# Performance work log

Hardware: AMD Instinct MI355X
Metric: run time of the kernel (lower is better)

The kernel has to match this reference:

```python
import jax, jax.numpy as jnp
import numpy as np

S, B, D, H, F = 1024, 8, 1024, 16, 4096
HD = D // H
EPS = 1e-5


def setup_inputs() -> dict:
    key = jax.random.key(0)
    ks = jax.random.split(key, 12)
    sc_d = 1.0 / np.sqrt(D)
    sc_f = 1.0 / np.sqrt(F)
    return {
        "src": jax.random.normal(ks[0], (S, B, D), jnp.float32),
        "in_proj_w": jax.random.uniform(ks[1], (3 * D, D), jnp.float32, -sc_d, sc_d),
        "in_proj_b": jnp.zeros((3 * D,), jnp.float32),
        "out_w": jax.random.uniform(ks[2], (D, D), jnp.float32, -sc_d, sc_d),
        "out_b": jnp.zeros((D,), jnp.float32),
        "w1": jax.random.uniform(ks[3], (F, D), jnp.float32, -sc_d, sc_d),
        "b1": jax.random.uniform(ks[4], (F,), jnp.float32, -sc_d, sc_d),
        "w2": jax.random.uniform(ks[5], (D, F), jnp.float32, -sc_f, sc_f),
        "b2": jax.random.uniform(ks[6], (D,), jnp.float32, -sc_f, sc_f),
        "g1": jnp.ones((D,), jnp.float32),
        "be1": jnp.zeros((D,), jnp.float32),
        "g2": jnp.ones((D,), jnp.float32),
        "be2": jnp.zeros((D,), jnp.float32),
    }


def _layer_norm(x, g, b):
    mu = jnp.mean(x, axis=-1, keepdims=True)
    var = jnp.mean(jnp.square(x - mu), axis=-1, keepdims=True)
    return (x - mu) * jax.lax.rsqrt(var + EPS) * g + b


def reference(src, in_proj_w, in_proj_b, out_w, out_b, w1, b1, w2, b2, g1, be1, g2, be2):
    wq, wk, wv = jnp.split(in_proj_w, 3, axis=0)
    bq, bk, bv = jnp.split(in_proj_b, 3, axis=0)
    scale = 1.0 / np.sqrt(HD)
    # src: [S, B, D] -> q/k/v: [S, B, H, HD]
    q = (src @ wq.T + bq).reshape(S, B, H, HD) * scale
    k = (src @ wk.T + bk).reshape(S, B, H, HD)
    v = (src @ wv.T + bv).reshape(S, B, H, HD)
    # full score matrix [B, H, S, S] (matches the unfused bmm/softmax/bmm)
    scores = jnp.einsum("sbhd,tbhd->bhst", q, k)
    attn = jax.nn.softmax(scores, axis=-1)
    ctx = jnp.einsum("bhst,tbhd->sbhd", attn, v).reshape(S, B, D)
    attn_out = ctx @ out_w.T + out_b
    x = _layer_norm(src + attn_out, g1, be1)
    ffn = jax.nn.relu(x @ w1.T + b1) @ w2.T + b2
    return _layer_norm(x + ffn, g2, be2)
```

## Files before the change

### kernel.cpp

```cpp
#include <hip/hip_runtime.h>
#include <hip/hip_bf16.h>
#include <stdint.h>

typedef __bf16 bf16x8 __attribute__((ext_vector_type(8)));
typedef __bf16 bf16x4 __attribute__((ext_vector_type(4)));
typedef float floatx4 __attribute__((ext_vector_type(4)));

typedef __attribute__((address_space(1))) void gvoid;
typedef __attribute__((address_space(3))) void lvoid;

__device__ __forceinline__ void async_load16(const __bf16* g, __bf16* l) {
  __builtin_amdgcn_global_load_lds((gvoid*)g, (lvoid*)l, 16, 0, 0);
}

__device__ __forceinline__ bf16x8 ld8(const float* p) {
  const floatx4 a = *(const floatx4*)p;
  const floatx4 b = *(const floatx4*)(p + 4);
  bf16x8 r;
  r[0] = (__bf16)a[0]; r[1] = (__bf16)a[1];
  r[2] = (__bf16)a[2]; r[3] = (__bf16)a[3];
  r[4] = (__bf16)b[0]; r[5] = (__bf16)b[1];
  r[6] = (__bf16)b[2]; r[7] = (__bf16)b[3];
  return r;
}

__global__ __launch_bounds__(256) void cvt_kernel(const float* __restrict__ in,
                                                  __bf16* __restrict__ out,
                                                  int n) {
  const int i = (blockIdx.x * 256 + threadIdx.x) * 8;
  if (i < n) *(bf16x8*)(out + i) = ld8(in + i);
}

template <int EPI>
__global__ __launch_bounds__(256, 2) void gemm_db64(
    const __bf16* __restrict__ A, const __bf16* __restrict__ Bt,
    const float* __restrict__ bias, const float* __restrict__ resf,
    const __bf16* __restrict__ resb, __bf16* __restrict__ o0,
    __bf16* __restrict__ o2, int M, int N, int K, int ldb) {
  __shared__ __align__(16) __bf16 As[2][2][128 * 32];
  __shared__ __align__(16) __bf16 Bs[2][2][128 * 32];
  const int tid = threadIdx.x;
  const int w = tid >> 6;
  const int lane = tid & 63;
  const int l16 = lane & 15;
  const int quad = lane >> 4;
  const int wm = (w & 1) * 64;
  const int wn = (w >> 1) * 64;
  const int bm = blockIdx.y * 128;
  const int bn = blockIdx.x * 128;

  floatx4 acc[4][4];
#pragma unroll
  for (int i = 0; i < 4; ++i)
#pragma unroll
    for (int j = 0; j < 4; ++j) acc[i][j] = (floatx4){0.f, 0.f, 0.f, 0.f};

  const int arow = lane >> 2, acol = (lane & 3) * 8;
  const __bf16* Ag = A + (int64_t)(bm + w * 32 + arow) * K + acol;
  const __bf16* Bg = Bt + (int64_t)(bn + w * 32 + arow) * ldb + acol;

  auto STAGE = [&](int b, int k0) {
#pragma unroll
    for (int kh = 0; kh < 2; ++kh) {
      __bf16* AsW = As[b][kh] + (w * 32) * 32;
      async_load16(Ag + k0 + kh * 32, AsW);
      async_load16(Ag + k0 + kh * 32 + 16 * K, AsW + 16 * 32);
      __bf16* BsW = Bs[b][kh] + (w * 32) * 32;
      async_load16(Bg + k0 + kh * 32, BsW);
      async_load16(Bg + k0 + kh * 32 + 16 * ldb, BsW + 16 * 32);
    }
  };

  STAGE(0, 0);
  __syncthreads();

  int cur = 0;
  for (int k0 = 0; k0 < K; k0 += 64) {
    if (k0 + 64 < K) STAGE(cur ^ 1, k0 + 64);
#pragma unroll
    for (int kh = 0; kh < 2; ++kh) {
      bf16x8 af[4], bfr[4];
#pragma unroll
      for (int i = 0; i < 4; ++i) {
        af[i] = *(const bf16x8*)(As[cur][kh] + (wm + i * 16 + l16) * 32 + quad * 8);
        bfr[i] = *(const bf16x8*)(Bs[cur][kh] + (wn + i * 16 + l16) * 32 + quad * 8);
      }
#pragma unroll
      for (int mi = 0; mi < 4; ++mi)
#pragma unroll
        for (int ni = 0; ni < 4; ++ni)
          acc[mi][ni] = __builtin_amdgcn_mfma_f32_16x16x32_bf16(
              af[mi], bfr[ni], acc[mi][ni], 0, 0, 0);
    }
    __syncthreads();
    cur ^= 1;
  }

#pragma unroll
  for (int ni = 0; ni < 4; ++ni) {
    const int gn = bn + wn + ni * 16 + l16;
    const float bv = (EPI == 3) ? 0.f : bias[gn];
#pragma unroll
    for (int mi = 0; mi < 4; ++mi) {
#pragma unroll
      for (int r = 0; r < 4; ++r) {
        const int gm = bm + wm + mi * 16 + quad * 4 + r;
        float v = acc[mi][ni][r] + bv;
        if (EPI == 0) {
          if (gn < 2048) {
            o0[(int64_t)gm * 2048 + gn] = (__bf16)(gn < 1024 ? v * 0.125f : v);
          } else {
            const int nn = gn - 2048, hh = nn >> 6, d = nn & 63;
            const int s = gm >> 3, b = gm & 7;
            o2[((b * 16 + hh) * 64 + d) * 1024 + s] = (__bf16)v;
          }
        } else {
          if (EPI == 1) v += resf[(int64_t)gm * N + gn];
          if (EPI == 3 || EPI == 4) v += (float)resb[(int64_t)gm * N + gn];
          if (EPI == 2) v = fmaxf(v, 0.f);
          o0[(int64_t)gm * N + gn] = (__bf16)v;
        }
      }
    }
  }
}

constexpr int BM = 128, BN = 128, BK = 32;

template <typename AT, int EPI>
__global__ __launch_bounds__(256, 2) void gemm_db(
    const AT* __restrict__ A, const __bf16* __restrict__ Bt,
    const float* __restrict__ bias, const float* __restrict__ resf,
    const __bf16* __restrict__ resb, __bf16* __restrict__ o0,
    __bf16* __restrict__ o2, int M, int N, int K, int ldb) {
  constexpr bool AF = sizeof(AT) == 4;
  __shared__ __align__(16) __bf16 As[2][BM * BK];
  __shared__ __align__(16) __bf16 Bs[2][BN * BK];
  const int tid = threadIdx.x;
  const int w = tid >> 6;
  const int lane = tid & 63;
  const int l16 = lane & 15;
  const int quad = lane >> 4;
  const int wm = (w & 1) * 64;
  const int wn = (w >> 1) * 64;
  const int bm = blockIdx.y * BM;
  const int bn = blockIdx.x * BN;

  floatx4 acc[4][4];
#pragma unroll
  for (int i = 0; i < 4; ++i)
#pragma unroll
    for (int j = 0; j < 4; ++j) acc[i][j] = (floatx4){0.f, 0.f, 0.f, 0.f};

  const int srow = tid >> 2, scol = (tid & 3) * 8;
  const int arow = lane >> 2, acol = (lane & 3) * 8;
  const AT* Ag;
  if constexpr (AF) Ag = A + (int64_t)(bm + srow) * K + scol;
  else Ag = A + (int64_t)(bm + w * 32 + arow) * K + acol;
  const __bf16* Bg = Bt + (int64_t)(bn + w * 32 + arow) * ldb + acol;

  bf16x8 a0, a1;
  if constexpr (AF) {
    a0 = ld8(Ag);
    a1 = ld8(Ag + (int64_t)64 * K);
    *(bf16x8*)(As[0] + tid * 8) = a0;
    *(bf16x8*)(As[0] + 2048 + tid * 8) = a1;
    if (BK < K) {
      a0 = ld8(Ag + BK);
      a1 = ld8(Ag + BK + (int64_t)64 * K);
    }
  } else {
    __bf16* AsW = As[0] + (w * 32) * BK;
    async_load16(Ag, AsW);
    async_load16(Ag + 16 * K, AsW + 16 * BK);
  }
  {
    __bf16* BsW = Bs[0] + (w * 32) * BK;
    async_load16(Bg, BsW);
    async_load16(Bg + 16 * ldb, BsW + 16 * BK);
  }
  __syncthreads();

  int cur = 0;
  for (int k0 = 0; k0 < K; k0 += BK) {
    const bool more = (k0 + BK) < K;
    if (more) {
      if constexpr (AF) {
        *(bf16x8*)(As[cur ^ 1] + tid * 8) = a0;
        *(bf16x8*)(As[cur ^ 1] + 2048 + tid * 8) = a1;
        if (k0 + 2 * BK < K) {
          a0 = ld8(Ag + k0 + 2 * BK);
          a1 = ld8(Ag + k0 + 2 * BK + (int64_t)64 * K);
        }
      } else {
        __bf16* AsW = As[cur ^ 1] + (w * 32) * BK;
        async_load16(Ag + k0 + BK, AsW);
        async_load16(Ag + k0 + BK + 16 * K, AsW + 16 * BK);
      }
      __bf16* BsW = Bs[cur ^ 1] + (w * 32) * BK;
      async_load16(Bg + k0 + BK, BsW);
      async_load16(Bg + k0 + BK + 16 * ldb, BsW + 16 * BK);
    }
    bf16x8 af[4], bfr[4];
#pragma unroll
    for (int i = 0; i < 4; ++i) {
      af[i] = *(const bf16x8*)(As[cur] + (wm + i * 16 + l16) * BK + quad * 8);
      bfr[i] = *(const bf16x8*)(Bs[cur] + (wn + i * 16 + l16) * BK + quad * 8);
    }
#pragma unroll
    for (int mi = 0; mi < 4; ++mi)
#pragma unroll
      for (int ni = 0; ni < 4; ++ni)
        acc[mi][ni] = __builtin_amdgcn_mfma_f32_16x16x32_bf16(
            af[mi], bfr[ni], acc[mi][ni], 0, 0, 0);
    __syncthreads();
    cur ^= 1;
  }

#pragma unroll
  for (int ni = 0; ni < 4; ++ni) {
    const int gn = bn + wn + ni * 16 + l16;
    const float bv = (EPI == 3) ? 0.f : bias[gn];
#pragma unroll
    for (int mi = 0; mi < 4; ++mi) {
#pragma unroll
      for (int r = 0; r < 4; ++r) {
        const int gm = bm + wm + mi * 16 + quad * 4 + r;
        float v = acc[mi][ni][r] + bv;
        if (EPI == 0) {
          if (gn < 2048) {
            o0[(int64_t)gm * 2048 + gn] = (__bf16)(gn < 1024 ? v * 0.125f : v);
          } else {
            const int nn = gn - 2048, hh = nn >> 6, d = nn & 63;
            const int s = gm >> 3, b = gm & 7;
            o2[((b * 16 + hh) * 64 + d) * 1024 + s] = (__bf16)v;
          }
        } else {
          if (EPI == 1) v += resf[(int64_t)gm * N + gn];
          if (EPI == 3 || EPI == 4) v += (float)resb[(int64_t)gm * N + gn];
          if (EPI == 2) v = fmaxf(v, 0.f);
          o0[(int64_t)gm * N + gn] = (__bf16)v;
        }
      }
    }
  }
}

__global__ __launch_bounds__(256) void attn_flash(
    const __bf16* __restrict__ qk, const __bf16* __restrict__ vT,
    __bf16* __restrict__ ctx) {
  constexpr int S = 1024, PSTR = 36;
  constexpr int ROWSTR = 8 * 2048;
  __shared__ __align__(16) __bf16 Kb[2][2048];
  __shared__ __align__(16) __bf16 Vb[2][2048];
  __shared__ __align__(16) __bf16 Pt[4][32 * PSTR];
  const int tid = threadIdx.x;
  const int w = tid >> 6;
  const int lane = tid & 63;
  const int l16 = lane & 15;
  const int quad = lane >> 4;
  const int bh = blockIdx.y, bidx = bh >> 4, h = bh & 15;
  const int qbase = blockIdx.x * 128 + w * 32;

  const __bf16* qp =
      qk + ((int64_t)(qbase + l16) * 8 + bidx) * 2048 + h * 64 + quad * 8;
  bf16x8 aq[2][2];
  aq[0][0] = *(const bf16x8*)qp;
  aq[0][1] = *(const bf16x8*)(qp + 32);
  aq[1][0] = *(const bf16x8*)(qp + 16 * ROWSTR);
  aq[1][1] = *(const bf16x8*)(qp + 16 * ROWSTR + 32);

  const __bf16* kg = qk + 1024 +
      ((int64_t)((w >> 1) * 16 + l16) * 8 + bidx) * 2048 + h * 64 +
      ((w & 1) * 4 + quad) * 8;
  const __bf16* vg =
      vT + ((int64_t)bh * 64 + w * 16 + l16) * 1024 + quad * 8;
  __bf16* pt = Pt[w];

  floatx4 o[2][4];
  float la[2][4];
#pragma unroll
  for (int rt = 0; rt < 2; ++rt)
#pragma unroll
    for (int j = 0; j < 4; ++j) {
      o[rt][j] = (floatx4){0.f, 0.f, 0.f, 0.f};
      la[rt][j] = 0.f;
    }

  async_load16(kg, Kb[0] + w * 512);
  async_load16(vg, Vb[0] + w * 512);
  int cur = 0;

  for (int t0 = 0; t0 < S; t0 += 32) {
    __syncthreads();
    if (t0 + 32 < S) {
      async_load16(kg + (int64_t)(t0 + 32) * ROWSTR, Kb[cur ^ 1] + w * 512);
      async_load16(vg + (t0 + 32), Vb[cur ^ 1] + w * 512);
    }

    bf16x8 kf[4], vv[4];
#pragma unroll
    for (int f = 0; f < 4; ++f) {
      kf[f] = *(const bf16x8*)(Kb[cur] + f * 512 + lane * 8);
      vv[f] = *(const bf16x8*)(Vb[cur] + f * 512 + lane * 8);
    }

    floatx4 s00 = (floatx4){0.f, 0.f, 0.f, 0.f};
    floatx4 s01 = (floatx4){0.f, 0.f, 0.f, 0.f};
    floatx4 s10 = (floatx4){0.f, 0.f, 0.f, 0.f};
    floatx4 s11 = (floatx4){0.f, 0.f, 0.f, 0.f};
    s00 = __builtin_amdgcn_mfma_f32_16x16x32_bf16(aq[0][0], kf[0], s00, 0, 0, 0);
    s00 = __builtin_amdgcn_mfma_f32_16x16x32_bf16(aq[0][1], kf[1], s00, 0, 0, 0);
    s01 = __builtin_amdgcn_mfma_f32_16x16x32_bf16(aq[0][0], kf[2], s01, 0, 0, 0);
    s01 = __builtin_amdgcn_mfma_f32_16x16x32_bf16(aq[0][1], kf[3], s01, 0, 0, 0);
    s10 = __builtin_amdgcn_mfma_f32_16x16x32_bf16(aq[1][0], kf[0], s10, 0, 0, 0);
    s10 = __builtin_amdgcn_mfma_f32_16x16x32_bf16(aq[1][1], kf[1], s10, 0, 0, 0);
    s11 = __builtin_amdgcn_mfma_f32_16x16x32_bf16(aq[1][0], kf[2], s11, 0, 0, 0);
    s11 = __builtin_amdgcn_mfma_f32_16x16x32_bf16(aq[1][1], kf[3], s11, 0, 0, 0);

#pragma unroll
    for (int r = 0; r < 4; ++r) {
      const int row0 = (quad * 4 + r) * PSTR;
      const float p00 = __expf(s00[r]);
      const float p01 = __expf(s01[r]);
      la[0][r] += p00 + p01;
      pt[row0 + l16] = (__bf16)p00;
      pt[row0 + 16 + l16] = (__bf16)p01;
      const int row1 = (16 + quad * 4 + r) * PSTR;
      const float p10 = __expf(s10[r]);
      const float p11 = __expf(s11[r]);
      la[1][r] += p10 + p11;
      pt[row1 + l16] = (__bf16)p10;
      pt[row1 + 16 + l16] = (__bf16)p11;
    }
    const bf16x8 pa0 = *(const bf16x8*)(pt + l16 * PSTR + quad * 8);
    const bf16x8 pa1 = *(const bf16x8*)(pt + (16 + l16) * PSTR + quad * 8);
#pragma unroll
    for (int j = 0; j < 4; ++j) {
      o[0][j] = __builtin_amdgcn_mfma_f32_16x16x32_bf16(pa0, vv[j], o[0][j], 0, 0, 0);
      o[1][j] = __builtin_amdgcn_mfma_f32_16x16x32_bf16(pa1, vv[j], o[1][j], 0, 0, 0);
    }
    cur ^= 1;
  }

#pragma unroll
  for (int rt = 0; rt < 2; ++rt)
#pragma unroll
    for (int r = 0; r < 4; ++r) {
      float s = la[rt][r];
      s += __shfl_xor(s, 1, 64);
      s += __shfl_xor(s, 2, 64);
      s += __shfl_xor(s, 4, 64);
      s += __shfl_xor(s, 8, 64);
      la[rt][r] = s;
    }
#pragma unroll
  for (int rt = 0; rt < 2; ++rt)
#pragma unroll
    for (int j = 0; j < 4; ++j)
#pragma unroll
      for (int r = 0; r < 4; ++r) {
        const int row = qbase + rt * 16 + quad * 4 + r;
        const int gm = row * 8 + bidx;
        ctx[(int64_t)gm * 1024 + h * 64 + j * 16 + l16] =
            (__bf16)(o[rt][j][r] / la[rt][r]);
      }
}

template <typename OutT>
__global__ __launch_bounds__(256) void ln_kernel(const __bf16* __restrict__ y,
                                                 const float* __restrict__ g,
                                                 const float* __restrict__ be,
                                                 OutT* __restrict__ out) {
  constexpr int D = 1024;
  const int row = blockIdx.x;
  const int tid = threadIdx.x;
  const __bf16* yr = y + (int64_t)row * D;
  const int c0 = tid * 4;
  const bf16x4 raw = *(const bf16x4*)(yr + c0);
  float v[4];
#pragma unroll
  for (int j = 0; j < 4; ++j) v[j] = (float)raw[j];
  float s = v[0] + v[1] + v[2] + v[3];
  float sq = v[0] * v[0] + v[1] * v[1] + v[2] * v[2] + v[3] * v[3];
#pragma unroll
  for (int off = 1; off < 64; off <<= 1) {
    s += __shfl_xor(s, off, 64);
    sq += __shfl_xor(sq, off, 64);
  }
  __shared__ float ls[4], lq[4];
  const int w = tid >> 6;
  if ((tid & 63) == 0) {
    ls[w] = s;
    lq[w] = sq;
  }
  __syncthreads();
  s = ls[0] + ls[1] + ls[2] + ls[3];
  sq = lq[0] + lq[1] + lq[2] + lq[3];
  const float mean = s * (1.f / D);
  const float var = sq * (1.f / D) - mean * mean;
  const float inv = rsqrtf(var + 1e-5f);
  const floatx4 gv = *(const floatx4*)(g + c0);
  const floatx4 bv = *(const floatx4*)(be + c0);
  if constexpr (sizeof(OutT) == 4) {
    floatx4 ov;
#pragma unroll
    for (int j = 0; j < 4; ++j) ov[j] = (v[j] - mean) * inv * gv[j] + bv[j];
    *(floatx4*)((float*)out + (int64_t)row * D + c0) = ov;
  } else {
    bf16x4 ov;
#pragma unroll
    for (int j = 0; j < 4; ++j)
      ov[j] = (__bf16)((v[j] - mean) * inv * gv[j] + bv[j]);
    *(bf16x4*)((__bf16*)out + (int64_t)row * D + c0) = ov;
  }
}

extern "C" void kernel_launch(void* const* d_in, const int* in_sizes, int n_in,
                              void* d_out, int out_size, void* d_ws,
                              size_t ws_size, hipStream_t stream) {
  const float* src = (const float*)d_in[0];
  const float* in_proj_w = (const float*)d_in[1];
  const float* in_proj_b = (const float*)d_in[2];
  const float* out_w = (const float*)d_in[3];
  const float* out_b = (const float*)d_in[4];
  const float* w1 = (const float*)d_in[5];
  const float* b1 = (const float*)d_in[6];
  const float* w2 = (const float*)d_in[7];
  const float* b2 = (const float*)d_in[8];
  const float* g1 = (const float*)d_in[9];
  const float* be1 = (const float*)d_in[10];
  const float* g2 = (const float*)d_in[11];
  const float* be2 = (const float*)d_in[12];

  char* ws = (char*)d_ws;
  char* out8 = (char*)d_out;
  __bf16* qkb = (__bf16*)ws;
  __bf16* vb = (__bf16*)out8;
  __bf16* ipwb = (__bf16*)(out8 + (16ull << 20));
  __bf16* srcb = (__bf16*)(ws + (32ull << 20));
  __bf16* ctxb = (__bf16*)(out8 + (16ull << 20));
  __bf16* owb = (__bf16*)ws;
  __bf16* yb = (__bf16*)(ws + (2ull << 20));
  __bf16* xb = (__bf16*)out8;

  const bool big = ws_size >= ((size_t)48 << 20);

  if (big) {
    __bf16* w1b = (__bf16*)(out8 + (16ull << 20));
    __bf16* w2b = (__bf16*)(out8 + (24ull << 20));
    __bf16* hb = (__bf16*)(ws + (16ull << 20));
    __bf16* zb = (__bf16*)ws;

    cvt_kernel<<<1536, 256, 0, stream>>>(in_proj_w, ipwb, 3 * 1024 * 1024);
    cvt_kernel<<<4096, 256, 0, stream>>>(src, srcb, 8 * 1024 * 1024);
    gemm_db64<0><<<dim3(24, 64), 256, 0, stream>>>(
        srcb, ipwb, in_proj_b, nullptr, nullptr, qkb, vb, 8192, 3072, 1024,
        1024);
    attn_flash<<<dim3(8, 128), 256, 0, stream>>>(qkb, vb, ctxb);
    cvt_kernel<<<512, 256, 0, stream>>>(out_w, owb, 1024 * 1024);
    gemm_db64<1><<<dim3(8, 64), 256, 0, stream>>>(
        ctxb, owb, out_b, src, nullptr, yb, nullptr, 8192, 1024, 1024, 1024);
    ln_kernel<__bf16><<<8192, 256, 0, stream>>>(yb, g1, be1, xb);
    cvt_kernel<<<2048, 256, 0, stream>>>(w1, w1b, 4 * 1024 * 1024);
    cvt_kernel<<<2048, 256, 0, stream>>>(w2, w2b, 4 * 1024 * 1024);
    for (int q = 0; q < 2; ++q) {
      gemm_db64<2><<<dim3(16, 64), 256, 0, stream>>>(
          xb, w1b + (int64_t)q * 2048 * 1024, b1 + q * 2048, nullptr, nullptr,
          hb, nullptr, 8192, 2048, 1024, 1024);
      if (q == 0)
        gemm_db64<4><<<dim3(8, 64), 256, 0, stream>>>(
            hb, w2b + q * 2048, b2, nullptr, xb, zb, nullptr, 8192, 1024, 2048,
            4096);
      else
        gemm_db64<3><<<dim3(8, 64), 256, 0, stream>>>(
            hb, w2b + q * 2048, nullptr, nullptr, zb, zb, nullptr, 8192, 1024,
            2048, 4096);
    }
    ln_kernel<float><<<8192, 256, 0, stream>>>(zb, g2, be2, (float*)d_out);
  } else {
    __bf16* w1b = (__bf16*)ws;
    __bf16* w2b = (__bf16*)(ws + (8ull << 20));
    __bf16* hb = (__bf16*)(out8 + (16ull << 20));
    __bf16* zb = (__bf16*)(ws + (16ull << 20));

    cvt_kernel<<<1536, 256, 0, stream>>>(in_proj_w, ipwb, 3 * 1024 * 1024);
    gemm_db<float, 0><<<dim3(24, 64), 256, 0, stream>>>(
        src, ipwb, in_proj_b, nullptr, nullptr, qkb, vb, 8192, 3072, 1024,
        1024);
    attn_flash<<<dim3(8, 128), 256, 0, stream>>>(qkb, vb, ctxb);
    cvt_kernel<<<512, 256, 0, stream>>>(out_w, owb, 1024 * 1024);
    gemm_db<__bf16, 1><<<dim3(8, 64), 256, 0, stream>>>(
        ctxb, owb, out_b, src, nullptr, yb, nullptr, 8192, 1024, 1024, 1024);
    ln_kernel<__bf16><<<8192, 256, 0, stream>>>(yb, g1, be1, xb);
    cvt_kernel<<<2048, 256, 0, stream>>>(w1, w1b, 4 * 1024 * 1024);
    cvt_kernel<<<2048, 256, 0, stream>>>(w2, w2b, 4 * 1024 * 1024);
    for (int qd = 0; qd < 4; ++qd) {
      gemm_db<__bf16, 2><<<dim3(8, 64), 256, 0, stream>>>(
          xb, w1b + (int64_t)qd * 1024 * 1024, b1 + qd * 1024, nullptr,
          nullptr, hb, nullptr, 8192, 1024, 1024, 1024);
      if (qd == 0)
        gemm_db<__bf16, 4><<<dim3(8, 64), 256, 0, stream>>>(
            hb, w2b + qd * 1024, b2, nullptr, xb, zb, nullptr, 8192, 1024,
            1024, 4096);
      else
        gemm_db<__bf16, 3><<<dim3(8, 64), 256, 0, stream>>>(
            hb, w2b + qd * 1024, nullptr, nullptr, zb, zb, nullptr, 8192, 1024,
            1024, 4096);
    }
    ln_kernel<float><<<8192, 256, 0, stream>>>(zb, g2, be2, (float*)d_out);
  }
}
```

Measured before the change: 540.8 us.

## Add 256x256-tile 8-wave GEMM with ping-pong scheduling for QKV and FFN1

Introduces a new GEMM kernel using 512 threads, 256x256 block tiles and 128KB of dynamic LDS. It double-buffers K-halves with async global-to-LDS loads interleaved between MFMA phases, using barriers and s_setprio to overlap loads and math. It is used for the QKV projection and the first FFN GEMM in place of the 128x128 kernel, aiming for more data reuse per tile and better MFMA utilisation. The costs are one block per CU, fewer blocks in the grid (384 and 256), and a scattered epilogue store pattern.

After: 555.9 us. 1.03x slower.

```diff
diff --git a/kernel.cpp b/kernel.cpp
--- a/kernel.cpp
+++ b/kernel.cpp
@@ -29,6 +29,161 @@
                                                   int n) {
   const int i = (blockIdx.x * 256 + threadIdx.x) * 8;
   if (i < n) *(bf16x8*)(out + i) = ld8(in + i);
+}
+
+#define MFMA16(AF, BFR, BASE)                                              \
+  _Pragma("unroll") for (int mi = 0; mi < 4; ++mi)                         \
+      _Pragma("unroll") for (int ni = 0; ni < 4; ++ni)                     \
+          acc[(BASE) + mi][ni] = __builtin_amdgcn_mfma_f32_16x16x32_bf16(  \
+              AF[mi], BFR[ni], acc[(BASE) + mi][ni], 0, 0, 0);
+
+template <int EPI>
+__global__ __launch_bounds__(512, 1) void gemm8p(
+    const __bf16* __restrict__ A, const __bf16* __restrict__ Bt,
+    const float* __restrict__ bias, const float* __restrict__ resf,
+    const __bf16* __restrict__ resb, __bf16* __restrict__ o0,
+    __bf16* __restrict__ o2, int M, int N, int K, int ldb) {
+  extern __shared__ __bf16 smem[];
+  const int tid = threadIdx.x;
+  const int w = tid >> 6, lane = tid & 63;
+  const int l16 = lane & 15, quad = lane >> 4;
+  const int wm = w >> 2, wn = w & 3;
+  const int bm = blockIdx.y * 256, bn = blockIdx.x * 256;
+  const int NT = K >> 6;
+
+  floatx4 acc[8][4];
+#pragma unroll
+  for (int i = 0; i < 8; ++i)
+#pragma unroll
+    for (int j = 0; j < 4; ++j) acc[i][j] = (floatx4){0.f, 0.f, 0.f, 0.f};
+
+  const int strow = tid >> 2, stcol = (tid & 3) * 8;
+  const __bf16* Ag = A + (int64_t)(bm + strow) * K + stcol;
+  const __bf16* Bg = Bt + (int64_t)(bn + strow) * ldb + stcol;
+  __bf16* AsB = smem;
+  __bf16* BsB = smem + 32768;
+
+  auto stageA = [&](int buf, int kh, int kofs) {
+    __bf16* d = AsB + (buf * 2 + kh) * 8192 + w * 512;
+    async_load16(Ag + kofs, d);
+    async_load16(Ag + kofs + (int64_t)128 * K, d + 4096);
+  };
+  auto stageB = [&](int buf, int kh, int kofs) {
+    __bf16* d = BsB + (buf * 2 + kh) * 8192 + w * 512;
+    async_load16(Bg + kofs, d);
+    async_load16(Bg + kofs + (int64_t)128 * ldb, d + 4096);
+  };
+
+  stageA(0, 0, 0);  stageB(0, 0, 0);
+  stageA(0, 1, 32); stageB(0, 1, 32);
+  stageA(1, 0, 64); stageB(1, 0, 64);
+  asm volatile("s_waitcnt vmcnt(8)" ::: "memory");
+  __builtin_amdgcn_s_barrier();
+  __builtin_amdgcn_sched_barrier(0);
+
+  for (int T = 0; T < NT; ++T) {
+    const int buf = T & 1;
+    const __bf16* Ap0 = AsB + (buf * 2 + 0) * 8192;
+    const __bf16* Ap1 = AsB + (buf * 2 + 1) * 8192;
+    const __bf16* Bp0 = BsB + (buf * 2 + 0) * 8192;
+    const __bf16* Bp1 = BsB + (buf * 2 + 1) * 8192;
+    bf16x8 af[4], bfr[4];
+
+#pragma unroll
+    for (int i = 0; i < 4; ++i)
+      bfr[i] = *(const bf16x8*)(Bp0 + (wn * 64 + i * 16 + l16) * 32 + quad * 8);
+#pragma unroll
+    for (int i = 0; i < 4; ++i)
+      af[i] = *(const bf16x8*)(Ap0 + (wm * 128 + i * 16 + l16) * 32 + quad * 8);
+    if (T + 1 < NT) stageA(buf ^ 1, 1, (T + 1) * 64 + 32);
+    __builtin_amdgcn_sched_barrier(0);
+    __builtin_amdgcn_s_barrier();
+    asm volatile("s_waitcnt lgkmcnt(0)" ::: "memory");
+    __builtin_amdgcn_sched_barrier(0);
+    __builtin_amdgcn_s_setprio(1);
+    MFMA16(af, bfr, 0)
+    __builtin_amdgcn_s_setprio(0);
+    __builtin_amdgcn_sched_barrier(0);
+    __builtin_amdgcn_s_barrier();
+
+#pragma unroll
+    for (int i = 0; i < 4; ++i)
+      af[i] = *(const bf16x8*)(Ap0 + (wm * 128 + 64 + i * 16 + l16) * 32 + quad * 8);
+    if (T + 1 < NT) stageB(buf ^ 1, 1, (T + 1) * 64 + 32);
+    __builtin_amdgcn_sched_barrier(0);
+    __builtin_amdgcn_s_barrier();
+    asm volatile("s_waitcnt lgkmcnt(0)" ::: "memory");
+    __builtin_amdgcn_sched_barrier(0);
+    __builtin_amdgcn_s_setprio(1);
+    MFMA16(af, bfr, 4)
+    __builtin_amdgcn_s_setprio(0);
+    __builtin_amdgcn_sched_barrier(0);
+    if (T == NT - 1) asm volatile("s_waitcnt vmcnt(0)" ::: "memory");
+    else asm volatile("s_waitcnt vmcnt(8)" ::: "memory");
+    __builtin_amdgcn_sched_barrier(0);
+    __builtin_amdgcn_s_barrier();
+
+#pragma unroll
+    for (int i = 0; i < 4; ++i)
+      bfr[i] = *(const bf16x8*)(Bp1 + (wn * 64 + i * 16 + l16) * 32 + quad * 8);
+#pragma unroll
+    for (int i = 0; i < 4; ++i)
+      af[i] = *(const bf16x8*)(Ap1 + (wm * 128 + i * 16 + l16) * 32 + quad * 8);
+    if (T + 2 < NT) stageA(buf, 0, (T + 2) * 64);
+    __builtin_amdgcn_sched_barrier(0);
+    __builtin_amdgcn_s_barrier();
+    asm volatile("s_waitcnt lgkmcnt(0)" ::: "memory");
+    __builtin_amdgcn_sched_barrier(0);
+    __builtin_amdgcn_s_setprio(1);
+    MFMA16(af, bfr, 0)
+    __builtin_amdgcn_s_setprio(0);
+    __builtin_amdgcn_sched_barrier(0);
+    __builtin_amdgcn_s_barrier();
+
+#pragma unroll
+    for (int i = 0; i < 4; ++i)
+      af[i] = *(const bf16x8*)(Ap1 + (wm * 128 + 64 + i * 16 + l16) * 32 + quad * 8);
+    if (T + 2 < NT) stageB(buf, 0, (T + 2) * 64);
+    __builtin_amdgcn_sched_barrier(0);
+    __builtin_amdgcn_s_barrier();
+    asm volatile("s_waitcnt lgkmcnt(0)" ::: "memory");
+    __builtin_amdgcn_sched_barrier(0);
+    __builtin_amdgcn_s_setprio(1);
+    MFMA16(af, bfr, 4)
+    __builtin_amdgcn_s_setprio(0);
+    __builtin_amdgcn_sched_barrier(0);
+    if (T == NT - 2) asm volatile("s_waitcnt vmcnt(4)" ::: "memory");
+    else if (T == NT - 1) asm volatile("s_waitcnt vmcnt(0)" ::: "memory");
+    else asm volatile("s_waitcnt vmcnt(8)" ::: "memory");
+    __builtin_amdgcn_sched_barrier(0);
+    __builtin_amdgcn_s_barrier();
+  }
+
+#pragma unroll
+  for (int ni = 0; ni < 4; ++ni) {
+    const int gn = bn + wn * 64 + ni * 16 + l16;
+    const float bv = bias[gn];
+#pragma unroll
+    for (int ai = 0; ai < 8; ++ai) {
+#pragma unroll
+      for (int r = 0; r < 4; ++r) {
+        const int gm = bm + wm * 128 + (ai >> 2) * 64 + (ai & 3) * 16 + quad * 4 + r;
+        float v = acc[ai][ni][r] + bv;
+        if (EPI == 0) {
+          if (gn < 2048) {
+            o0[(int64_t)gm * 2048 + gn] = (__bf16)(gn < 1024 ? v * 0.125f : v);
+          } else {
+            const int nn = gn - 2048, hh = nn >> 6, d = nn & 63;
+            const int s = gm >> 3, b = gm & 7;
+            o2[((b * 16 + hh) * 64 + d) * 1024 + s] = (__bf16)v;
+          }
+        } else {
+          v = fmaxf(v, 0.f);
+          o0[(int64_t)gm * N + gn] = (__bf16)v;
+        }
+      }
+    }
+  }
 }
 
 template <int EPI>
@@ -452,9 +607,14 @@
     __bf16* hb = (__bf16*)(ws + (16ull << 20));
     __bf16* zb = (__bf16*)ws;
 
+    hipFuncSetAttribute(reinterpret_cast<const void*>(&gemm8p<0>),
+                        hipFuncAttributeMaxDynamicSharedMemorySize, 131072);
+    hipFuncSetAttribute(reinterpret_cast<const void*>(&gemm8p<2>),
+                        hipFuncAttributeMaxDynamicSharedMemorySize, 131072);
+
     cvt_kernel<<<1536, 256, 0, stream>>>(in_proj_w, ipwb, 3 * 1024 * 1024);
     cvt_kernel<<<4096, 256, 0, stream>>>(src, srcb, 8 * 1024 * 1024);
-    gemm_db64<0><<<dim3(24, 64), 256, 0, stream>>>(
+    gemm8p<0><<<dim3(12, 32), 512, 131072, stream>>>(
         srcb, ipwb, in_proj_b, nullptr, nullptr, qkb, vb, 8192, 3072, 1024,
         1024);
     attn_flash<<<dim3(8, 128), 256, 0, stream>>>(qkb, vb, ctxb);
@@ -465,7 +625,7 @@
     cvt_kernel<<<2048, 256, 0, stream>>>(w1, w1b, 4 * 1024 * 1024);
     cvt_kernel<<<2048, 256, 0, stream>>>(w2, w2b, 4 * 1024 * 1024);
     for (int q = 0; q < 2; ++q) {
-      gemm_db64<2><<<dim3(16, 64), 256, 0, stream>>>(
+      gemm8p<2><<<dim3(8, 32), 512, 131072, stream>>>(
           xb, w1b + (int64_t)q * 2048 * 1024, b1 + q * 2048, nullptr, nullptr,
           hb, nullptr, 8192, 2048, 1024, 1024);
       if (q == 0)
```
